# Kernel optimization log

Hardware: AMD Instinct MI355X
Metric: run time of the kernel (lower is better)

The kernel has to match this reference:

```python
import jax, jax.numpy as jnp
import numpy as np

N = 50000      # nodes
E = 800000     # edges
H = 128        # hidden_dim
EF = 16        # edge_feat_dim
EIN = 2 * H + 1 + EF  # edge MLP input dim = 273


def setup_inputs() -> dict:
    key = jax.random.key(0)
    ks = jax.random.split(key, 20)
    s = 0.05
    return {
        "h": jax.random.normal(ks[0], (N, H), jnp.float32),
        "x": jax.random.normal(ks[1], (N, 3), jnp.float32),
        "edge_attr": jax.random.normal(ks[2], (E, EF), jnp.float32),
        # edge MLP: Linear(EIN,H) -> SiLU -> Linear(H,H) -> SiLU
        "we_w1": jax.random.normal(ks[3], (EIN, H), jnp.float32) * s,
        "we_b1": jnp.zeros((H,), jnp.float32),
        "we_w2": jax.random.normal(ks[4], (H, H), jnp.float32) * s,
        "we_b2": jnp.zeros((H,), jnp.float32),
        # coord MLP: Linear(H,H) -> SiLU -> Linear(H,1, bias=False), tiny init
        "wc_w1": jax.random.normal(ks[5], (H, H), jnp.float32) * s,
        "wc_b1": jnp.zeros((H,), jnp.float32),
        "wc_w2": jax.random.normal(ks[6], (H, 1), jnp.float32) * 0.001,
        # node MLP: Linear(2H,H) -> SiLU -> Linear(H,H)
        "wn_w1": jax.random.normal(ks[7], (2 * H, H), jnp.float32) * s,
        "wn_b1": jnp.zeros((H,), jnp.float32),
        "wn_w2": jax.random.normal(ks[8], (H, H), jnp.float32) * s,
        "wn_b2": jnp.zeros((H,), jnp.float32),
        # layer norm
        "ln_g": jnp.ones((H,), jnp.float32),
        "ln_b": jnp.zeros((H,), jnp.float32),
        "edge_index": jax.random.randint(ks[9], (2, E), 0, N, dtype=jnp.int32),
    }


def reference(h, x, edge_attr, we_w1, we_b1, we_w2, we_b2,
              wc_w1, wc_b1, wc_w2, wn_w1, wn_b1, wn_w2, wn_b2,
              ln_g, ln_b, edge_index):
    row, col = edge_index[0], edge_index[1]
    n = h.shape[0]

    coord_diff = x[row] - x[col]                         # [E, 3]
    dist_sq = jnp.sum(coord_diff ** 2, axis=-1, keepdims=True)  # [E, 1]

    edge_input = jnp.concatenate([h[row], h[col], dist_sq, edge_attr], axis=-1)  # [E, EIN]
    m_ij = jax.nn.silu(edge_input @ we_w1 + we_b1)
    m_ij = jax.nn.silu(m_ij @ we_w2 + we_b2)             # [E, H]

    # coordinate update
    coord_w = jnp.tanh(jax.nn.silu(m_ij @ wc_w1 + wc_b1) @ wc_w2)  # [E, 1]
    dist = jnp.sqrt(dist_sq + 1e-8)
    weighted_diff = (coord_diff / dist) * coord_w        # [E, 3]
    x_update = jax.ops.segment_sum(weighted_diff, row, num_segments=n)
    degree = jax.ops.segment_sum(jnp.ones((row.shape[0], 1), x.dtype), row, num_segments=n)
    degree = jnp.maximum(degree, 1.0)
    x_out = x + x_update / degree

    # node update with residual + layernorm
    m_i = jax.ops.segment_sum(m_ij, row, num_segments=n)  # [N, H]
    node_input = jnp.concatenate([h, m_i], axis=-1)       # [N, 2H]
    h_res = h + (jax.nn.silu(node_input @ wn_w1 + wn_b1) @ wn_w2 + wn_b2)

    mu = jnp.mean(h_res, axis=-1, keepdims=True)
    var = jnp.var(h_res, axis=-1, keepdims=True)
    h_out = (h_res - mu) * jax.lax.rsqrt(var + 1e-5) * ln_g + ln_b
    return (h_out, x_out)
```

## Files before the change

### kernel.cpp

```cpp
#include <hip/hip_runtime.h>

typedef unsigned short u16;
typedef unsigned int u32;
using short8 = __attribute__((ext_vector_type(8))) short;
using f32x4  = __attribute__((ext_vector_type(4))) float;
using u32x4  = __attribute__((ext_vector_type(4))) u32;

#define N_CNT 50000
#define E_CNT 800000
#define EB_CNT 400000

__device__ __forceinline__ u16 f2bf(float f) {
  u32 u = __builtin_bit_cast(u32, f);
  u += 0x7fffu + ((u >> 16) & 1u);
  return (u16)(u >> 16);
}
__device__ __forceinline__ float bf2f(u16 v) {
  u32 u = ((u32)v) << 16;
  return __builtin_bit_cast(float, u);
}
__device__ __forceinline__ short8 pack8(f32x4 v0, f32x4 v1) {
  short8 r;
#pragma unroll
  for (int j = 0; j < 4; ++j) r[j] = (short)f2bf(v0[j]);
#pragma unroll
  for (int j = 0; j < 4; ++j) r[4 + j] = (short)f2bf(v1[j]);
  return r;
}
__device__ __forceinline__ float siluf(float v) {
  return __fdividef(v, 1.f + __expf(-v));
}

__global__ void k_wf(const float* __restrict__ w1, const float* __restrict__ w2,
                     const float* __restrict__ wc1, const float* __restrict__ wn1,
                     const float* __restrict__ wn2,
                     u16* __restrict__ wef, u16* __restrict__ w1abf,
                     u16* __restrict__ wnf) {
  int idx = blockIdx.x * 256 + threadIdx.x;
  int i = idx & 7, l = (idx >> 3) & 63;
  int kb = 8 * (l >> 4) + i;
  int n16 = l & 15;
  if (idx < 4096) {
    int t = idx >> 9;
    int k = kb, n = 16 * t + n16;
    wef[idx] = (k < 17) ? f2bf(w1[(256 + k) * 128 + n]) : (u16)0;
  } else if (idx < 20480) {
    int u = idx - 4096, rest = u >> 9;
    int s = rest & 3, t = rest >> 2;
    wef[idx] = f2bf(w2[(32 * s + kb) * 128 + 16 * t + n16]);
  } else if (idx < 36864) {
    int u = idx - 20480, rest = u >> 9;
    int s = rest & 3, t = rest >> 2;
    wef[idx] = f2bf(wc1[(32 * s + kb) * 128 + 16 * t + n16]);
  } else if (idx < 69632) {
    int u = idx - 36864, rest = u >> 9;
    int s = rest & 3, t = rest >> 2;
    int k = 32 * s + kb, n = 16 * t + n16;
    float v = (n < 128) ? w1[k * 128 + n] : w1[(128 + k) * 128 + (n - 128)];
    w1abf[u] = f2bf(v);
  } else if (idx < 102400) {
    int u = idx - 69632, rest = u >> 9;
    int s = rest & 7, t = rest >> 3;
    wnf[u] = f2bf(wn1[(32 * s + kb) * 128 + 16 * t + n16]);
  } else if (idx < 118784) {
    int u = idx - 102400, rest = u >> 9;
    int s = rest & 3, t = rest >> 2;
    wnf[32768 + u] = f2bf(wn2[(32 * s + kb) * 128 + 16 * t + n16]);
  }
}

__global__ __launch_bounds__(256)
void k_hp(const float* __restrict__ h, const u16* __restrict__ w1abf,
          const float* __restrict__ b1v, u16* __restrict__ hp) {
  extern __shared__ char smem[];
  u16* wl = (u16*)smem;
  const int tid = threadIdx.x;
  {
    const u32x4* src = reinterpret_cast<const u32x4*>(w1abf);
    u32x4* dst = reinterpret_cast<u32x4*>(smem);
    for (int i2 = tid; i2 < 4096; i2 += 256) dst[i2] = src[i2];
  }
  __syncthreads();
  const int w = tid >> 6, lane = tid & 63;
  const int g = lane >> 4, c15 = lane & 15;
  float b1r[8];
#pragma unroll
  for (int t = 0; t < 8; ++t) b1r[t] = b1v[t * 16 + c15];

  int wt = blockIdx.x * 4 + w;
  if (wt >= 3125) return;
  int nbase = wt * 16;
  int nr = nbase + c15;
  short8 af[4];
#pragma unroll
  for (int s = 0; s < 4; ++s) {
    const float* p = h + nr * 128 + s * 32 + g * 8;
    af[s] = pack8(*reinterpret_cast<const f32x4*>(p),
                  *reinterpret_cast<const f32x4*>(p + 4));
  }
  f32x4 acc[16];
#pragma unroll
  for (int t = 0; t < 16; ++t) acc[t] = (f32x4){0.f, 0.f, 0.f, 0.f};
#pragma unroll
  for (int s = 0; s < 4; ++s) {
#pragma unroll
    for (int t = 0; t < 16; ++t) {
      short8 bf = *reinterpret_cast<const short8*>(wl + ((t * 4 + s) * 64 + lane) * 8);
      acc[t] = __builtin_amdgcn_mfma_f32_16x16x32_bf16(af[s], bf, acc[t], 0, 0, 0);
    }
  }
#pragma unroll
  for (int t = 0; t < 16; ++t) {
    float bb = (t < 8) ? b1r[t] : 0.f;
    int col = t * 16 + c15;
#pragma unroll
    for (int i = 0; i < 4; ++i)
      hp[(size_t)(nbase + g * 4 + i) * 256 + col] = f2bf(acc[t][i] + bb);
  }
}

__global__ void k_deg(const int* __restrict__ eidx, int* __restrict__ degs) {
  int e = blockIdx.x * 256 + threadIdx.x;
  int b = (e >= EB_CNT) ? 1 : 0;
  atomicAdd(&degs[b * N_CNT + eidx[e]], 1);
}

__global__ void k_bsum(const int* __restrict__ degs, int* __restrict__ bsum) {
  int bid = blockIdx.x;
  int batch = bid / 98, chunk = bid % 98;
  const int* deg = degs + batch * N_CNT;
  int b0 = chunk * 512 + threadIdx.x;
  int b1 = b0 + 256;
  int v = ((b0 < N_CNT) ? deg[b0] : 0) + ((b1 < N_CNT) ? deg[b1] : 0);
#pragma unroll
  for (int m = 1; m <= 32; m <<= 1) v += __shfl_xor(v, m, 64);
  __shared__ int ws[4];
  if ((threadIdx.x & 63) == 0) ws[threadIdx.x >> 6] = v;
  __syncthreads();
  if (threadIdx.x == 0) bsum[bid] = ws[0] + ws[1] + ws[2] + ws[3];
}

__global__ void k_mid(const int* __restrict__ bsum, int* __restrict__ boff,
                      int* __restrict__ rps) {
  int wv = threadIdx.x >> 6, lane = threadIdx.x & 63;
  if (wv >= 2) return;
  const int* bs = bsum + wv * 98;
  int* bo = boff + wv * 98;
  int carry = 0;
  for (int base = 0; base < 98; base += 64) {
    int idx = base + lane;
    int v = (idx < 98) ? bs[idx] : 0;
    int inc = v;
#pragma unroll
    for (int d = 1; d <= 32; d <<= 1) {
      int u = __shfl_up(inc, d, 64);
      if (lane >= d) inc += u;
    }
    if (idx < 98) bo[idx] = carry + inc - v;
    carry += __shfl(inc, 63, 64);
  }
  if (lane == 0) rps[wv * (N_CNT + 1) + N_CNT] = EB_CNT;
}

__global__ void k_rp(const int* __restrict__ degs, const int* __restrict__ boff,
                     int* __restrict__ rps) {
  int bid = blockIdx.x;
  int batch = bid / 98, chunk = bid % 98;
  const int* deg = degs + batch * N_CNT;
  int* rp = rps + batch * (N_CNT + 1);
  int i0 = chunk * 512 + 2 * threadIdx.x, i1 = i0 + 1;
  int a = (i0 < N_CNT) ? deg[i0] : 0;
  int b = (i1 < N_CNT) ? deg[i1] : 0;
  int s = a + b, lane = threadIdx.x & 63, wv = threadIdx.x >> 6;
  int inc = s;
#pragma unroll
  for (int d = 1; d <= 32; d <<= 1) {
    int u = __shfl_up(inc, d, 64);
    if (lane >= d) inc += u;
  }
  __shared__ int ws2[4];
  if (lane == 63) ws2[wv] = inc;
  __syncthreads();
  int woff = 0;
  for (int k = 0; k < wv; ++k) woff += ws2[k];
  int excl = boff[bid] + woff + inc - s;
  if (i0 < N_CNT) rp[i0] = excl;
  if (i1 < N_CNT) rp[i1] = excl + a;
}

__global__ void k_scatter(const int* __restrict__ eidx, const int* __restrict__ rps,
                          int* __restrict__ curs, int* __restrict__ pos) {
  int e = blockIdx.x * 256 + threadIdx.x;
  int b = (e >= EB_CNT) ? 1 : 0;
  int r = eidx[e];
  int p = atomicAdd(&curs[b * N_CNT + r], 1);
  pos[e] = rps[b * (N_CNT + 1) + r] + p;
}

__global__ __launch_bounds__(1024, 4)
void egnn_edge4(const u16* __restrict__ hp, const float* __restrict__ xc,
                const float* __restrict__ ea, const int* __restrict__ eidx,
                const int* __restrict__ pos, const u16* __restrict__ wef,
                const float* __restrict__ b2v, const float* __restrict__ bc1v,
                const float* __restrict__ wc2v,
                u16* __restrict__ m_ij, float* __restrict__ x_acc, int ebase0) {
  extern __shared__ char smem[];
  const int tid = threadIdx.x;
  {
    const u32x4* src = reinterpret_cast<const u32x4*>(wef);
    u32x4* dst = reinterpret_cast<u32x4*>(smem);
    for (int i2 = tid; i2 < 4608; i2 += 1024) dst[i2] = src[i2];
  }
  const int w = tid >> 6, lane = tid & 63;
  const int g = lane >> 4, c15 = lane & 15;
  const int e4 = lane >> 2, q4 = lane & 3;
  const u16* w1tf = (const u16*)smem;
  const u16* w2f  = (const u16*)(smem + 8192);
  const u16* wc1f = (const u16*)(smem + 40960);
  u16* atail = (u16*)(smem + 73728 + w * 1024);
  u16* mbuf  = (u16*)(smem + 90112 + w * 4352);
  *reinterpret_cast<u32x4*>((char*)atail + lane * 16) = (u32x4){0, 0, 0, 0};
  __syncthreads();

  float b2r[8], bc1r[8], wc2r[8];
#pragma unroll
  for (int t = 0; t < 8; ++t) {
    b2r[t]  = b2v[t * 16 + c15];
    bc1r[t] = bc1v[t * 16 + c15];
    wc2r[t] = wc2v[t * 16 + c15];
  }

  for (int bt = blockIdx.x; bt < 1563; bt += gridDim.x) {
    int wt = bt * 16 + w;
    if (wt >= 25000) continue;
    const int eb = ebase0 + wt * 16;
    int r_v = 0, c_v = 0, p_v = 0;
    if (lane < 16) {
      int gi = eb + lane;
      r_v = eidx[gi]; c_v = eidx[E_CNT + gi]; p_v = pos[gi];
      float d0 = xc[3 * r_v + 0] - xc[3 * c_v + 0];
      float d1 = xc[3 * r_v + 1] - xc[3 * c_v + 1];
      float d2 = xc[3 * r_v + 2] - xc[3 * c_v + 2];
      float dsq = d0 * d0 + d1 * d1 + d2 * d2;
      f32x4 cd = {d0, d1, d2, dsq};
      *reinterpret_cast<f32x4*>(mbuf + lane * 136 + 128) = cd;
    }
    int re = __shfl(r_v, c15, 64);
    int ce = __shfl(c_v, c15, 64);
    int pc = __shfl(p_v, c15, 64);
    short8 ga[4], gb[4];
    {
      const u16* pa = hp + (size_t)re * 256 + g * 8;
      const u16* pb = hp + (size_t)ce * 256 + 128 + g * 8;
#pragma unroll
      for (int s = 0; s < 4; ++s) ga[s] = *reinterpret_cast<const short8*>(pa + s * 32);
#pragma unroll
      for (int s = 0; s < 4; ++s) gb[s] = *reinterpret_cast<const short8*>(pb + s * 32);
    }
    {
      u16* row = atail + e4 * 32;
      f32x4 eav = *reinterpret_cast<const f32x4*>(ea + (size_t)(eb + e4) * 16 + q4 * 4);
#pragma unroll
      for (int jj = 0; jj < 4; ++jj)
        row[1 + q4 * 4 + jj] = f2bf(eav[jj]);
      if (q4 == 0) {
        float dq = reinterpret_cast<const float*>(mbuf + e4 * 136 + 128)[3];
        row[0] = f2bf(dq);
      }
    }
    short8 af8 = *reinterpret_cast<const short8*>(atail + c15 * 32 + g * 8);
    f32x4 acc[8];
#pragma unroll
    for (int t = 0; t < 8; ++t) acc[t] = (f32x4){0.f, 0.f, 0.f, 0.f};
#pragma unroll
    for (int t = 0; t < 8; ++t) {
      short8 bf = *reinterpret_cast<const short8*>(w1tf + (t * 64 + lane) * 8);
      acc[t] = __builtin_amdgcn_mfma_f32_16x16x32_bf16(af8, bf, acc[t], 0, 0, 0);
    }
#pragma unroll
    for (int t = 0; t < 8; ++t) {
      int col = t * 16 + c15;
#pragma unroll
      for (int i = 0; i < 4; ++i)
        mbuf[(g * 4 + i) * 136 + col] = f2bf(acc[t][i]);
    }
    short8 a2[4];
#pragma unroll
    for (int s = 0; s < 4; ++s) {
      short8 tl = *reinterpret_cast<const short8*>(mbuf + c15 * 136 + s * 32 + g * 8);
      short8 o;
#pragma unroll
      for (int j = 0; j < 8; ++j) {
        float v = bf2f((u16)tl[j]) + bf2f((u16)ga[s][j]) + bf2f((u16)gb[s][j]);
        o[j] = (short)f2bf(siluf(v));
      }
      a2[s] = o;
    }
    f32x4 acc2[8];
#pragma unroll
    for (int t = 0; t < 8; ++t) acc2[t] = (f32x4){0.f, 0.f, 0.f, 0.f};
#pragma unroll
    for (int s = 0; s < 4; ++s) {
#pragma unroll
      for (int t = 0; t < 8; ++t) {
        short8 bf = *reinterpret_cast<const short8*>(w2f + ((t * 4 + s) * 64 + lane) * 8);
        acc2[t] = __builtin_amdgcn_mfma_f32_16x16x32_bf16(a2[s], bf, acc2[t], 0, 0, 0);
      }
    }
#pragma unroll
    for (int t = 0; t < 8; ++t) {
      int col = t * 16 + c15;
#pragma unroll
      for (int i = 0; i < 4; ++i)
        mbuf[(g * 4 + i) * 136 + col] = f2bf(siluf(acc2[t][i] + b2r[t]));
    }
    short8 a3[4];
#pragma unroll
    for (int s = 0; s < 4; ++s) {
      a3[s] = *reinterpret_cast<const short8*>(mbuf + c15 * 136 + s * 32 + g * 8);
      *reinterpret_cast<short8*>(m_ij + (size_t)pc * 128 + s * 32 + g * 8) = a3[s];
    }
    f32x4 acc3[8];
#pragma unroll
    for (int t = 0; t < 8; ++t) acc3[t] = (f32x4){0.f, 0.f, 0.f, 0.f};
#pragma unroll
    for (int s = 0; s < 4; ++s) {
#pragma unroll
      for (int t = 0; t < 8; ++t) {
        short8 bf = *reinterpret_cast<const short8*>(wc1f + ((t * 4 + s) * 64 + lane) * 8);
        acc3[t] = __builtin_amdgcn_mfma_f32_16x16x32_bf16(a3[s], bf, acc3[t], 0, 0, 0);
      }
    }
    float p4[4] = {0.f, 0.f, 0.f, 0.f};
#pragma unroll
    for (int t = 0; t < 8; ++t)
#pragma unroll
      for (int i = 0; i < 4; ++i)
        p4[i] += siluf(acc3[t][i] + bc1r[t]) * wc2r[t];
#pragma unroll
    for (int m = 1; m <= 8; m <<= 1) {
#pragma unroll
      for (int i = 0; i < 4; ++i) p4[i] += __shfl_xor(p4[i], m, 64);
    }
    int rr[4];
#pragma unroll
    for (int i = 0; i < 4; ++i) rr[i] = __shfl(r_v, g * 4 + i, 64);
    if (c15 == 0) {
#pragma unroll
      for (int i = 0; i < 4; ++i) {
        f32x4 cd = *reinterpret_cast<const f32x4*>(mbuf + (g * 4 + i) * 136 + 128);
        float fac = rsqrtf(cd[3] + 1e-8f) * tanhf(p4[i]);
        atomicAdd(&x_acc[rr[i] * 4 + 0], cd[0] * fac);
        atomicAdd(&x_acc[rr[i] * 4 + 1], cd[1] * fac);
        atomicAdd(&x_acc[rr[i] * 4 + 2], cd[2] * fac);
      }
    }
  }
}

template <int ACC>
__global__ __launch_bounds__(256)
void k_gather(const u16* __restrict__ m_ij, const int* __restrict__ rp,
              float* __restrict__ m_i) {
  const int tid = threadIdx.x, w = tid >> 6, lane = tid & 63;
  const int grp = lane >> 4, c16 = lane & 15;
  int node = blockIdx.x * 4 + w;
  int beg = rp[node], end = rp[node + 1];
  float a[8] = {0.f, 0.f, 0.f, 0.f, 0.f, 0.f, 0.f, 0.f};
  for (int j = beg + grp; j < end; j += 4) {
    short8 v = *reinterpret_cast<const short8*>(m_ij + (size_t)j * 128 + c16 * 8);
#pragma unroll
    for (int k = 0; k < 8; ++k) a[k] += bf2f((u16)v[k]);
  }
#pragma unroll
  for (int k = 0; k < 8; ++k) {
    a[k] += __shfl_xor(a[k], 16, 64);
    a[k] += __shfl_xor(a[k], 32, 64);
  }
  if (grp == 0) {
    float* dst = m_i + node * 128 + c16 * 8;
    if (ACC) {
      f32x4 o0 = *reinterpret_cast<const f32x4*>(dst);
      f32x4 o1 = *reinterpret_cast<const f32x4*>(dst + 4);
#pragma unroll
      for (int k = 0; k < 4; ++k) { o0[k] += a[k]; o1[k] += a[4 + k]; }
      *reinterpret_cast<f32x4*>(dst) = o0;
      *reinterpret_cast<f32x4*>(dst + 4) = o1;
    } else {
      f32x4 o0 = {a[0], a[1], a[2], a[3]};
      f32x4 o1 = {a[4], a[5], a[6], a[7]};
      *reinterpret_cast<f32x4*>(dst) = o0;
      *reinterpret_cast<f32x4*>(dst + 4) = o1;
    }
  }
}

__global__ __launch_bounds__(256)
void egnn_node2(const float* __restrict__ h, const float* __restrict__ m_i,
                const u16* __restrict__ wnf,
                const float* __restrict__ bn1, const float* __restrict__ bn2,
                const float* __restrict__ lng, const float* __restrict__ lnb,
                float* __restrict__ h_out) {
  __shared__ u16 mbuf_all[4][2176];
  const int tid = threadIdx.x, w = tid >> 6, lane = tid & 63;
  const int g = lane >> 4, c15 = lane & 15;
  u16* mbuf = mbuf_all[w];
  const u16* wn1f = wnf;
  const u16* wn2f = wnf + 32768;

  float bn1r[8], bn2r[8], lngr[8], lnbr[8];
#pragma unroll
  for (int t = 0; t < 8; ++t) {
    bn1r[t] = bn1[t * 16 + c15];
    bn2r[t] = bn2[t * 16 + c15];
    lngr[t] = lng[t * 16 + c15];
    lnbr[t] = lnb[t * 16 + c15];
  }

  int wt = blockIdx.x * 4 + w;
  if (wt >= 3125) return;
  int nbase = wt * 16;
  int nr = nbase + c15;
  short8 af[8];
#pragma unroll
  for (int s = 0; s < 4; ++s) {
    const float* p = h + nr * 128 + s * 32 + g * 8;
    af[s] = pack8(*reinterpret_cast<const f32x4*>(p),
                  *reinterpret_cast<const f32x4*>(p + 4));
  }
#pragma unroll
  for (int s = 0; s < 4; ++s) {
    const float* p = m_i + nr * 128 + s * 32 + g * 8;
    af[4 + s] = pack8(*reinterpret_cast<const f32x4*>(p),
                      *reinterpret_cast<const f32x4*>(p + 4));
  }
  f32x4 acc[8];
#pragma unroll
  for (int t = 0; t < 8; ++t) acc[t] = (f32x4){0.f, 0.f, 0.f, 0.f};
#pragma unroll
  for (int s = 0; s < 8; ++s) {
#pragma unroll
    for (int t = 0; t < 8; ++t) {
      short8 bf = *reinterpret_cast<const short8*>(wn1f + ((t * 8 + s) * 64 + lane) * 8);
      acc[t] = __builtin_amdgcn_mfma_f32_16x16x32_bf16(af[s], bf, acc[t], 0, 0, 0);
    }
  }
#pragma unroll
  for (int t = 0; t < 8; ++t) {
    int col = t * 16 + c15;
#pragma unroll
    for (int i = 0; i < 4; ++i)
      mbuf[(g * 4 + i) * 136 + col] = f2bf(siluf(acc[t][i] + bn1r[t]));
  }
  short8 a2[4];
#pragma unroll
  for (int s = 0; s < 4; ++s)
    a2[s] = *reinterpret_cast<const short8*>(mbuf + c15 * 136 + s * 32 + g * 8);
  f32x4 acc2[8];
#pragma unroll
  for (int t = 0; t < 8; ++t) acc2[t] = (f32x4){0.f, 0.f, 0.f, 0.f};
#pragma unroll
  for (int s = 0; s < 4; ++s) {
#pragma unroll
    for (int t = 0; t < 8; ++t) {
      short8 bf = *reinterpret_cast<const short8*>(wn2f + ((t * 4 + s) * 64 + lane) * 8);
      acc2[t] = __builtin_amdgcn_mfma_f32_16x16x32_bf16(a2[s], bf, acc2[t], 0, 0, 0);
    }
  }
  float vres[8][4];
  float s1[4] = {0.f, 0.f, 0.f, 0.f}, s2[4] = {0.f, 0.f, 0.f, 0.f};
#pragma unroll
  for (int t = 0; t < 8; ++t)
#pragma unroll
    for (int i = 0; i < 4; ++i) {
      int n = nbase + g * 4 + i;
      float v = acc2[t][i] + bn2r[t] + h[n * 128 + t * 16 + c15];
      vres[t][i] = v; s1[i] += v; s2[i] += v * v;
    }
#pragma unroll
  for (int m = 1; m <= 8; m <<= 1) {
#pragma unroll
    for (int i = 0; i < 4; ++i) {
      s1[i] += __shfl_xor(s1[i], m, 64);
      s2[i] += __shfl_xor(s2[i], m, 64);
    }
  }
  float mu[4], rstd[4];
#pragma unroll
  for (int i = 0; i < 4; ++i) {
    mu[i] = s1[i] * (1.0f / 128.0f);
    float var = s2[i] * (1.0f / 128.0f) - mu[i] * mu[i];
    rstd[i] = rsqrtf(var + 1e-5f);
  }
#pragma unroll
  for (int t = 0; t < 8; ++t)
#pragma unroll
    for (int i = 0; i < 4; ++i) {
      int n = nbase + g * 4 + i;
      h_out[n * 128 + t * 16 + c15] =
          (vres[t][i] - mu[i]) * rstd[i] * lngr[t] + lnbr[t];
    }
}

__global__ void egnn_xout(const float* __restrict__ x, const float* __restrict__ x_acc,
                          const int* __restrict__ degs, float* __restrict__ xo) {
  int n = blockIdx.x * 256 + threadIdx.x;
  if (n < N_CNT) {
    float dg = fmaxf((float)(degs[n] + degs[N_CNT + n]), 1.0f);
    xo[n * 3 + 0] = x[n * 3 + 0] + x_acc[n * 4 + 0] / dg;
    xo[n * 3 + 1] = x[n * 3 + 1] + x_acc[n * 4 + 1] / dg;
    xo[n * 3 + 2] = x[n * 3 + 2] + x_acc[n * 4 + 2] / dg;
  }
}

extern "C" void kernel_launch(void* const* d_in, const int* in_sizes, int n_in,
                              void* d_out, int out_size, void* d_ws, size_t ws_size,
                              hipStream_t stream) {
  const float* h     = (const float*)d_in[0];
  const float* x     = (const float*)d_in[1];
  const float* ea    = (const float*)d_in[2];
  const float* we_w1 = (const float*)d_in[3];
  const float* we_b1 = (const float*)d_in[4];
  const float* we_w2 = (const float*)d_in[5];
  const float* we_b2 = (const float*)d_in[6];
  const float* wc_w1 = (const float*)d_in[7];
  const float* wc_b1 = (const float*)d_in[8];
  const float* wc_w2 = (const float*)d_in[9];
  const float* wn_w1 = (const float*)d_in[10];
  const float* wn_b1 = (const float*)d_in[11];
  const float* wn_w2 = (const float*)d_in[12];
  const float* wn_b2 = (const float*)d_in[13];
  const float* ln_g  = (const float*)d_in[14];
  const float* ln_b  = (const float*)d_in[15];
  const int* eidx    = (const int*)d_in[16];
  float* out = (float*)d_out;
  char* ws = (char*)d_ws;

  u16* wef    = (u16*)(ws);
  u16* w1abf  = (u16*)(ws + 73728);
  u16* wnf    = (u16*)(ws + 139264);
  u16* hp     = (u16*)(ws + 237568);
  float* m_i  = (float*)(ws + 25837568);
  float* xacc = (float*)(ws + 51437568);
  int* degs   = (int*)(ws + 52237568);
  int* curs   = (int*)(ws + 52637568);
  int* rps    = (int*)(ws + 53037568);
  int* pos    = (int*)(ws + 53437584);
  int* bsum   = (int*)(ws + 56637584);
  int* boff   = (int*)(ws + 56638384);
  u16* m_ij   = (u16*)(ws + 56639200);

  k_wf<<<464, 256, 0, stream>>>(we_w1, we_w2, wc_w1, wn_w1, wn_w2, wef, w1abf, wnf);

  hipFuncSetAttribute(reinterpret_cast<const void*>(k_hp),
                      hipFuncAttributeMaxDynamicSharedMemorySize, 65536);
  k_hp<<<782, 256, 65536, stream>>>(h, w1abf, we_b1, hp);

  hipMemsetAsync(ws + 51437568, 0, 1600000, stream);
  k_deg<<<3125, 256, 0, stream>>>(eidx, degs);
  k_bsum<<<196, 256, 0, stream>>>(degs, bsum);
  k_mid<<<1, 128, 0, stream>>>(bsum, boff, rps);
  k_rp<<<196, 256, 0, stream>>>(degs, boff, rps);
  k_scatter<<<3125, 256, 0, stream>>>(eidx, rps, curs, pos);

  hipFuncSetAttribute(reinterpret_cast<const void*>(egnn_edge4),
                      hipFuncAttributeMaxDynamicSharedMemorySize, 159744);
  egnn_edge4<<<256, 1024, 159744, stream>>>(hp, x, ea, eidx, pos, wef,
                                            we_b2, wc_b1, wc_w2, m_ij, xacc, 0);
  k_gather<0><<<12500, 256, 0, stream>>>(m_ij, rps, m_i);
  egnn_edge4<<<256, 1024, 159744, stream>>>(hp, x, ea, eidx, pos, wef,
                                            we_b2, wc_b1, wc_w2, m_ij, xacc, EB_CNT);
  k_gather<1><<<12500, 256, 0, stream>>>(m_ij, rps + (N_CNT + 1), m_i);

  egnn_node2<<<782, 256, 0, stream>>>(h, m_i, wnf, wn_b1, wn_b2, ln_g, ln_b, out);
  egnn_xout<<<196, 256, 0, stream>>>(x, xacc, degs, out + 6400000);
}
```

Before: 455.3 us.

## Software-pipeline edge gathers by prefetching next tile during MFMA compute

Restructures the persistent edge-kernel loop so that the indices, coordinates, edge attributes and h-projection rows for the next tile are loaded while the current tile runs its MFMA layers. This is meant to hide the latency of the random global gathers behind matrix compute. In exchange it raises register pressure (double-buffered ga/gb, eav and coordinate values) in a 1024-thread kernel with launch_bounds(1024,4), which risks spills or fewer resident waves. Out-of-range next tiles are clamped to tile 0 so the extra loads stay in bounds.

```diff
diff --git a/kernel.cpp b/kernel.cpp
--- a/kernel.cpp
+++ b/kernel.cpp
@@ -198,7 +198,7 @@
 }
 
 __global__ __launch_bounds__(1024, 4)
-void egnn_edge4(const u16* __restrict__ hp, const float* __restrict__ xc,
+void egnn_edge6(const u16* __restrict__ hp, const float* __restrict__ xc,
                 const float* __restrict__ ea, const int* __restrict__ eidx,
                 const int* __restrict__ pos, const u16* __restrict__ wef,
                 const float* __restrict__ b2v, const float* __restrict__ bc1v,
@@ -230,36 +230,43 @@
     wc2r[t] = wc2v[t * 16 + c15];
   }
 
-  for (int bt = blockIdx.x; bt < 1563; bt += gridDim.x) {
+  int bt = blockIdx.x;
+  int r_v = 0, c_v = 0, p_v = 0;
+  float xr0 = 0.f, xr1 = 0.f, xr2 = 0.f, xq0 = 0.f, xq1 = 0.f, xq2 = 0.f;
+  f32x4 eav;
+  short8 ga[4], gb[4];
+  {
     int wt = bt * 16 + w;
-    if (wt >= 25000) continue;
-    const int eb = ebase0 + wt * 16;
-    int r_v = 0, c_v = 0, p_v = 0;
+    int eb = ebase0 + wt * 16;
     if (lane < 16) {
       int gi = eb + lane;
       r_v = eidx[gi]; c_v = eidx[E_CNT + gi]; p_v = pos[gi];
-      float d0 = xc[3 * r_v + 0] - xc[3 * c_v + 0];
-      float d1 = xc[3 * r_v + 1] - xc[3 * c_v + 1];
-      float d2 = xc[3 * r_v + 2] - xc[3 * c_v + 2];
+      xr0 = xc[3 * r_v + 0]; xr1 = xc[3 * r_v + 1]; xr2 = xc[3 * r_v + 2];
+      xq0 = xc[3 * c_v + 0]; xq1 = xc[3 * c_v + 1]; xq2 = xc[3 * c_v + 2];
+    }
+    eav = *reinterpret_cast<const f32x4*>(ea + (size_t)(eb + e4) * 16 + q4 * 4);
+    int re = __shfl(r_v, c15, 64);
+    int ce = __shfl(c_v, c15, 64);
+    const u16* pa = hp + (size_t)re * 256 + g * 8;
+    const u16* pb = hp + (size_t)ce * 256 + 128 + g * 8;
+#pragma unroll
+    for (int s = 0; s < 4; ++s) ga[s] = *reinterpret_cast<const short8*>(pa + s * 32);
+#pragma unroll
+    for (int s = 0; s < 4; ++s) gb[s] = *reinterpret_cast<const short8*>(pb + s * 32);
+  }
+
+  for (; bt < 1563; bt += gridDim.x) {
+    int wt = bt * 16 + w;
+    if (wt >= 25000) continue;
+    if (lane < 16) {
+      float d0 = xr0 - xq0, d1 = xr1 - xq1, d2 = xr2 - xq2;
       float dsq = d0 * d0 + d1 * d1 + d2 * d2;
       f32x4 cd = {d0, d1, d2, dsq};
       *reinterpret_cast<f32x4*>(mbuf + lane * 136 + 128) = cd;
     }
-    int re = __shfl(r_v, c15, 64);
-    int ce = __shfl(c_v, c15, 64);
     int pc = __shfl(p_v, c15, 64);
-    short8 ga[4], gb[4];
-    {
-      const u16* pa = hp + (size_t)re * 256 + g * 8;
-      const u16* pb = hp + (size_t)ce * 256 + 128 + g * 8;
-#pragma unroll
-      for (int s = 0; s < 4; ++s) ga[s] = *reinterpret_cast<const short8*>(pa + s * 32);
-#pragma unroll
-      for (int s = 0; s < 4; ++s) gb[s] = *reinterpret_cast<const short8*>(pb + s * 32);
-    }
     {
       u16* row = atail + e4 * 32;
-      f32x4 eav = *reinterpret_cast<const f32x4*>(ea + (size_t)(eb + e4) * 16 + q4 * 4);
 #pragma unroll
       for (int jj = 0; jj < 4; ++jj)
         row[1 + q4 * 4 + jj] = f2bf(eav[jj]);
@@ -268,6 +275,16 @@
         row[0] = f2bf(dq);
       }
     }
+    int btn = bt + gridDim.x;
+    int wtn = btn * 16 + w;
+    int wtn2 = (btn < 1563 && wtn < 25000) ? wtn : 0;
+    int ebn = ebase0 + wtn2 * 16;
+    int r_n = 0, c_n = 0, p_n = 0;
+    if (lane < 16) {
+      int gin = ebn + lane;
+      r_n = eidx[gin]; c_n = eidx[E_CNT + gin]; p_n = pos[gin];
+    }
+    f32x4 eav_n = *reinterpret_cast<const f32x4*>(ea + (size_t)(ebn + e4) * 16 + q4 * 4);
     short8 af8 = *reinterpret_cast<const short8*>(atail + c15 * 32 + g * 8);
     f32x4 acc[8];
 #pragma unroll
@@ -306,6 +323,22 @@
         short8 bf = *reinterpret_cast<const short8*>(w2f + ((t * 4 + s) * 64 + lane) * 8);
         acc2[t] = __builtin_amdgcn_mfma_f32_16x16x32_bf16(a2[s], bf, acc2[t], 0, 0, 0);
       }
+    }
+    float xr0n = 0.f, xr1n = 0.f, xr2n = 0.f, xq0n = 0.f, xq1n = 0.f, xq2n = 0.f;
+    if (lane < 16) {
+      xr0n = xc[3 * r_n + 0]; xr1n = xc[3 * r_n + 1]; xr2n = xc[3 * r_n + 2];
+      xq0n = xc[3 * c_n + 0]; xq1n = xc[3 * c_n + 1]; xq2n = xc[3 * c_n + 2];
+    }
+    int ren = __shfl(r_n, c15, 64);
+    int cen = __shfl(c_n, c15, 64);
+    short8 ga_n[4], gb_n[4];
+    {
+      const u16* pa = hp + (size_t)ren * 256 + g * 8;
+      const u16* pb = hp + (size_t)cen * 256 + 128 + g * 8;
+#pragma unroll
+      for (int s = 0; s < 4; ++s) ga_n[s] = *reinterpret_cast<const short8*>(pa + s * 32);
+#pragma unroll
+      for (int s = 0; s < 4; ++s) gb_n[s] = *reinterpret_cast<const short8*>(pb + s * 32);
     }
 #pragma unroll
     for (int t = 0; t < 8; ++t) {
@@ -355,6 +388,12 @@
         atomicAdd(&x_acc[rr[i] * 4 + 2], cd[2] * fac);
       }
     }
+    r_v = r_n; c_v = c_n; p_v = p_n;
+    xr0 = xr0n; xr1 = xr1n; xr2 = xr2n;
+    xq0 = xq0n; xq1 = xq1n; xq2 = xq2n;
+    eav = eav_n;
+#pragma unroll
+    for (int s = 0; s < 4; ++s) { ga[s] = ga_n[s]; gb[s] = gb_n[s]; }
   }
 }
 
@@ -563,12 +602,12 @@
   k_rp<<<196, 256, 0, stream>>>(degs, boff, rps);
   k_scatter<<<3125, 256, 0, stream>>>(eidx, rps, curs, pos);
 
-  hipFuncSetAttribute(reinterpret_cast<const void*>(egnn_edge4),
+  hipFuncSetAttribute(reinterpret_cast<const void*>(egnn_edge6),
                       hipFuncAttributeMaxDynamicSharedMemorySize, 159744);
-  egnn_edge4<<<256, 1024, 159744, stream>>>(hp, x, ea, eidx, pos, wef,
+  egnn_edge6<<<256, 1024, 159744, stream>>>(hp, x, ea, eidx, pos, wef,
                                             we_b2, wc_b1, wc_w2, m_ij, xacc, 0);
   k_gather<0><<<12500, 256, 0, stream>>>(m_ij, rps, m_i);
-  egnn_edge4<<<256, 1024, 159744, stream>>>(hp, x, ea, eidx, pos, wef,
+  egnn_edge6<<<256, 1024, 159744, stream>>>(hp, x, ea, eidx, pos, wef,
                                             we_b2, wc_b1, wc_w2, m_ij, xacc, EB_CNT);
   k_gather<1><<<12500, 256, 0, stream>>>(m_ij, rps + (N_CNT + 1), m_i);
 
```

Result: slower. 474.0 us (+4.1%).
